# Kernel optimization log

Measured on AMD Instinct MI355X. Metric: run time of the kernel, lower is better.

The kernel has to match this reference:

```python
import jax, jax.numpy as jnp
import numpy as np

N_NODES = 100000
N_EDGES = 3200000
N_GRAPHS = 512
IN_DIM = 128
H1, H2 = 32, 64
OUT_DIM = 1
LN_EPS = 1e-5


def setup_inputs() -> dict:
    key = jax.random.key(0)
    ks = jax.random.split(key, 12)
    x = jax.random.normal(ks[0], (N_NODES, IN_DIM), dtype=jnp.float32)
    edge_index = jax.random.randint(ks[1], (2, N_EDGES), 0, N_NODES, dtype=jnp.int64)
    batch = jnp.sort(jax.random.randint(ks[2], (N_NODES,), 0, N_GRAPHS, dtype=jnp.int64))
    def lin(k, fi, fo):
        s = 1.0 / np.sqrt(fi)
        return jax.random.uniform(k, (fi, fo), minval=-s, maxval=s, dtype=jnp.float32)
    params = {
        'W1': lin(ks[3], IN_DIM, H1), 'b1': jnp.zeros((H1,), jnp.float32),
        'g1': jnp.ones((H1,), jnp.float32), 'be1': jnp.zeros((H1,), jnp.float32),
        'W2': lin(ks[4], H1, H2), 'b2': jnp.zeros((H2,), jnp.float32),
        'g2': jnp.ones((H2,), jnp.float32), 'be2': jnp.zeros((H2,), jnp.float32),
        'Wc1': lin(ks[5], H2, 32), 'bc1': jnp.zeros((32,), jnp.float32),
        'Wc2': lin(ks[6], 32, OUT_DIM), 'bc2': jnp.zeros((OUT_DIM,), jnp.float32),
    }
    return {'x': x, 'edge_index': edge_index, 'batch': batch, **params}


def _gcn_norm(edge_index, n):
    # add self loops (PyG GCNConv default)
    loop = jnp.arange(n, dtype=edge_index.dtype)
    src = jnp.concatenate([edge_index[0], loop])
    dst = jnp.concatenate([edge_index[1], loop])
    deg = jax.ops.segment_sum(jnp.ones_like(dst, dtype=jnp.float32), dst, num_segments=n)
    dinv = jnp.where(deg > 0, 1.0 / jnp.sqrt(deg), 0.0)
    norm = dinv[src] * dinv[dst]  # [E+N]
    return src, dst, norm


def _gcn_conv(x, src, dst, norm, W, b, n):
    h = x @ W                                    # tiny GEMM
    msg = h[src] * norm[:, None]                 # gather + scale (memory-bound)
    agg = jax.ops.segment_sum(msg, dst, num_segments=n)  # scatter-add
    return agg + b


def _layernorm(x, g, b):
    mu = jnp.mean(x, axis=-1, keepdims=True)
    var = jnp.mean(jnp.square(x - mu), axis=-1, keepdims=True)
    return (x - mu) * jax.lax.rsqrt(var + LN_EPS) * g + b


def reference(x, edge_index, batch, W1, b1, g1, be1, W2, b2, g2, be2, Wc1, bc1, Wc2, bc2):
    n = x.shape[0]
    src, dst, norm = _gcn_norm(edge_index, n)
    # layer 1: GCNConv -> LayerNorm -> ReLU (dropout = identity in eval)
    h = jax.nn.relu(_layernorm(_gcn_conv(x, src, dst, norm, W1, b1, n), g1, be1))
    # layer 2
    h = jax.nn.relu(_layernorm(_gcn_conv(h, src, dst, norm, W2, b2, n), g2, be2))
    # global mean pool over graphs
    sums = jax.ops.segment_sum(h, batch, num_segments=N_GRAPHS)
    cnts = jax.ops.segment_sum(jnp.ones((n,), h.dtype), batch, num_segments=N_GRAPHS)
    pooled = sums / jnp.maximum(cnts, 1.0)[:, None]  # [G, H2]
    # classifier MLP
    z = jax.nn.relu(pooled @ Wc1 + bc1)
    return z @ Wc2 + bc2
```

## Files before the change

kernel.cpp:

```cpp
#include <hip/hip_runtime.h>
#include <hip/hip_fp16.h>

#define CAP 10240

__global__ __launch_bounds__(1024) void k_fused1(const int* __restrict__ ei,
                                                 const float* __restrict__ x,
                                                 const float* __restrict__ W1,
                                                 const int* __restrict__ batch,
                                                 int* __restrict__ gcnt,
                                                 int* __restrict__ bucketed,
                                                 __half* __restrict__ hs,
                                                 int* __restrict__ gstart,
                                                 int nA, int nG1, int NB,
                                                 int n, int E, int G) {
    __shared__ __align__(16) char smem[32768];
    int tid = threadIdx.x;
    int bid = blockIdx.x;
    if (bid < nA) {
        int* hist = (int*)smem;
        int* base = (int*)(smem + 2048);
        const int* src = ei;
        const int* dst = ei + E;
        for (int i = tid; i < NB; i += 1024) hist[i] = 0;
        __syncthreads();
        int e0 = bid * 8192;
        int e1 = min(e0 + 8192, E);
        for (int e = e0 + tid; e < e1; e += 1024)
            atomicAdd(&hist[dst[e] >> 8], 1);
        __syncthreads();
        for (int i = tid; i < NB; i += 1024) {
            int h = hist[i];
            base[i] = h ? atomicAdd(&gcnt[i], h) : 0;
            hist[i] = 0;
        }
        __syncthreads();
        for (int e = e0 + tid; e < e1; e += 1024) {
            int d = dst[e], s = src[e];
            int b = d >> 8;
            int p = base[b] + atomicAdd(&hist[b], 1);
            if (p < CAP) bucketed[(size_t)b * CAP + p] = (s << 8) | (d & 255);
        }
    } else if (bid < nA + nG1) {
        float* Ws = (float*)smem;
        float* xs = (float*)(smem + 16384);
        int gb = bid - nA;
        const float4* W4 = (const float4*)W1;
        ((float4*)Ws)[tid] = W4[tid];
        int rbase = gb * 32;
        const float4* x4 = (const float4*)x;
        {
            int r = rbase + (tid >> 5);
            ((float4*)xs)[tid] = (r < n) ? x4[(size_t)r * 32 + (tid & 31)]
                                         : make_float4(0.f, 0.f, 0.f, 0.f);
        }
        __syncthreads();
        int row = tid >> 5, col = tid & 31;
        float acc = 0.0f;
#pragma unroll
        for (int k = 0; k < 128; k++) acc += xs[row * 128 + k] * Ws[k * 32 + col];
        int r = rbase + row;
        if (r < n) hs[(size_t)r * 32 + col] = __float2half(acc);
    } else {
        int i = (bid - nA - nG1) * 1024 + tid;
        if (i > n) return;
        if (i == 0) {
            for (int g = 0; g <= batch[0]; g++) gstart[g] = 0;
        } else if (i == n) {
            for (int g = batch[n - 1] + 1; g <= G; g++) gstart[g] = n;
        } else {
            int b = batch[i], p = batch[i - 1];
            for (int g = p + 1; g <= b; g++) gstart[g] = i;
        }
    }
}

__global__ __launch_bounds__(512) void k_bucketB(const int* __restrict__ bucketed,
                                                 const int* __restrict__ gcnt,
                                                 int* __restrict__ csr,
                                                 int* __restrict__ offs,
                                                 int* __restrict__ deg,
                                                 float* __restrict__ dinv,
                                                 __half* __restrict__ hs, int n) {
    __shared__ int hist[256], scan_a[256], scan_b[256];
    __shared__ float sdinv[256];
    int b = blockIdx.x;
    int tid = threadIdx.x;
    int cnt = min(gcnt[b], CAP);
    int base = b * CAP;
    const int* ent = bucketed + (size_t)b * CAP;
    if (tid < 256) hist[tid] = 0;
    __syncthreads();
    for (int i = tid; i < cnt; i += 512) atomicAdd(&hist[ent[i] & 255], 1);
    __syncthreads();
    int h = (tid < 256) ? hist[tid] : 0;
    if (tid < 256) scan_a[tid] = h;
    __syncthreads();
    int* cur = scan_a;
    int* nxt = scan_b;
    for (int off = 1; off < 256; off <<= 1) {
        if (tid < 256) nxt[tid] = cur[tid] + ((tid >= off) ? cur[tid - off] : 0);
        __syncthreads();
        int* tmp = cur; cur = nxt; nxt = tmp;
    }
    if (tid < 256) {
        int ex = cur[tid] - h;
        float dv = rsqrtf((float)(h + 1));
        sdinv[tid] = dv;
        int node = b * 256 + tid;
        if (node < n) {
            offs[node] = base + ex;
            deg[node] = h;
            dinv[node] = dv;
        }
        hist[tid] = ex;
    }
    __syncthreads();
    for (int i = tid; i < cnt; i += 512) {
        int v = ent[i];
        int p = atomicAdd(&hist[v & 255], 1);
        csr[base + p] = v >> 8;
    }
    float4* hsv = (float4*)hs;
#pragma unroll
    for (int p = 0; p < 2; p++) {
        int idx = p * 512 + tid;
        int nl = idx >> 2, cg = idx & 3;
        int node = b * 256 + nl;
        if (node < n) {
            float dv = sdinv[nl];
            float4 raw = hsv[(size_t)node * 4 + cg];
            __half2* h2 = (__half2*)&raw;
            __half2 o[4];
#pragma unroll
            for (int j = 0; j < 4; j++) {
                float2 f = __half22float2(h2[j]);
                o[j] = __floats2half2_rn(f.x * dv, f.y * dv);
            }
            hsv[(size_t)node * 4 + cg] = *(const float4*)o;
        }
    }
}

template <bool DO_LN>
__global__ __launch_bounds__(256) void k_gather(const __half* __restrict__ hs,
                                                const int* __restrict__ csr,
                                                const int* __restrict__ offs,
                                                const int* __restrict__ deg,
                                                const float* __restrict__ dinv,
                                                const float* __restrict__ b,
                                                const float* __restrict__ g,
                                                const float* __restrict__ be,
                                                __half* __restrict__ out, int n) {
    int wave = threadIdx.x >> 6;
    int lane = threadIdx.x & 63;
    int row = blockIdx.x * 4 + wave;
    if (row >= n) return;
    int nb = lane >> 2;
    int cg = lane & 3;
    int base = offs[row];
    int dg = deg[row];
    const float4* hsv = (const float4*)hs;
    float acc[8];
#pragma unroll
    for (int j = 0; j < 8; j++) acc[j] = 0.f;
    int nfull = dg & ~15;
    for (int it = 0; it < nfull; it += 16) {
        int s = csr[base + it + nb];
        float4 raw = hsv[(size_t)s * 4 + cg];
        const __half2* h2 = (const __half2*)&raw;
#pragma unroll
        for (int j = 0; j < 4; j++) {
            float2 f = __half22float2(h2[j]);
            acc[2 * j]     += f.x;
            acc[2 * j + 1] += f.y;
        }
    }
    if (nfull + nb < dg) {
        int s = csr[base + nfull + nb];
        float4 raw = hsv[(size_t)s * 4 + cg];
        const __half2* h2 = (const __half2*)&raw;
#pragma unroll
        for (int j = 0; j < 4; j++) {
            float2 f = __half22float2(h2[j]);
            acc[2 * j]     += f.x;
            acc[2 * j + 1] += f.y;
        }
    }
#pragma unroll
    for (int m = 4; m <= 32; m <<= 1)
#pragma unroll
        for (int j = 0; j < 8; j++) acc[j] += __shfl_xor(acc[j], m, 64);
    float dv = dinv[row];
    float4 sraw = hsv[(size_t)row * 4 + cg];
    const __half2* sh2 = (const __half2*)&sraw;
    float a[8];
#pragma unroll
    for (int j = 0; j < 4; j++) {
        float2 f = __half22float2(sh2[j]);
        a[2 * j]     = (acc[2 * j]     + f.x) * dv;
        a[2 * j + 1] = (acc[2 * j + 1] + f.y) * dv;
    }
    if (DO_LN) {
        int c0 = cg * 8;
        float s = 0.f;
#pragma unroll
        for (int j = 0; j < 8; j++) { a[j] += b[c0 + j]; s += a[j]; }
#pragma unroll
        for (int m = 1; m <= 2; m <<= 1) s += __shfl_xor(s, m, 64);
        float mu = s * (1.0f / 32.0f);
        float v2 = 0.f;
#pragma unroll
        for (int j = 0; j < 8; j++) { a[j] -= mu; v2 += a[j] * a[j]; }
#pragma unroll
        for (int m = 1; m <= 2; m <<= 1) v2 += __shfl_xor(v2, m, 64);
        float inv = rsqrtf(v2 * (1.0f / 32.0f) + 1e-5f);
#pragma unroll
        for (int j = 0; j < 8; j++)
            a[j] = fmaxf(a[j] * inv * g[c0 + j] + be[c0 + j], 0.f) * dv;
    }
    if (nb == 0) {
        __half2 o[4];
#pragma unroll
        for (int j = 0; j < 4; j++) o[j] = __floats2half2_rn(a[2 * j], a[2 * j + 1]);
        ((float4*)out)[(size_t)row * 4 + cg] = *(const float4*)o;
    }
}

__global__ __launch_bounds__(512) void k_pool_cls(const __half* __restrict__ agg2,
                                                  const float* __restrict__ W2,
                                                  const float* __restrict__ b2,
                                                  const float* __restrict__ g2,
                                                  const float* __restrict__ be2,
                                                  const int* __restrict__ gstart,
                                                  const float* __restrict__ Wc1,
                                                  const float* __restrict__ bc1,
                                                  const float* __restrict__ Wc2,
                                                  const float* __restrict__ bc2,
                                                  float* __restrict__ out) {
    __shared__ float Ws[32 * 64];
    __shared__ float red[8 * 64];
    int tid = threadIdx.x;
    for (int i = tid; i < 32 * 64; i += 512) Ws[i] = W2[i];
    int g = blockIdx.x;
    int r0 = gstart[g], r1 = gstart[g + 1];
    int wave = tid >> 6, lane = tid & 63;
    float pacc = 0.0f;
    __syncthreads();
    for (int row = r0 + wave; row < r1; row += 8) {
        const float4* a4 = (const float4*)(agg2 + (size_t)row * 32);
        float4 r4[4];
#pragma unroll
        for (int q = 0; q < 4; q++) r4[q] = a4[q];
        const __half2* ah = (const __half2*)r4;
        float acc = b2[lane];
#pragma unroll
        for (int k2 = 0; k2 < 16; k2++) {
            float2 f = __half22float2(ah[k2]);
            acc += f.x * Ws[(2 * k2) * 64 + lane] + f.y * Ws[(2 * k2 + 1) * 64 + lane];
        }
        float s = acc;
#pragma unroll
        for (int m = 32; m >= 1; m >>= 1) s += __shfl_xor(s, m, 64);
        float mu = s * (1.0f / 64.0f);
        float d = acc - mu;
        float v = d * d;
#pragma unroll
        for (int m = 32; m >= 1; m >>= 1) v += __shfl_xor(v, m, 64);
        float val = d * rsqrtf(v * (1.0f / 64.0f) + 1e-5f) * g2[lane] + be2[lane];
        pacc += fmaxf(val, 0.0f);
    }
    red[wave * 64 + lane] = pacc;
    __syncthreads();
    if (wave == 0) {
        float p = 0.f;
#pragma unroll
        for (int w = 0; w < 8; w++) p += red[w * 64 + lane];
        p *= 1.0f / fmaxf((float)(r1 - r0), 1.0f);
        red[lane] = p;
    }
    __syncthreads();
    if (wave == 0 && lane < 32) {
        float zs = bc1[lane];
#pragma unroll
        for (int k = 0; k < 64; k++) zs += red[k] * Wc1[k * 32 + lane];
        float o = fmaxf(zs, 0.0f) * Wc2[lane];
#pragma unroll
        for (int m = 16; m >= 1; m >>= 1) o += __shfl_xor(o, m, 64);
        if (lane == 0) out[g] = o + bc2[0];
    }
}


extern "C" void kernel_launch(void* const* d_in, const int* in_sizes, int n_in,
                              void* d_out, int out_size, void* d_ws, size_t ws_size,
                              hipStream_t stream) {
    const float* x     = (const float*)d_in[0];
    const int*   ei    = (const int*)d_in[1];
    const int*   batch = (const int*)d_in[2];
    const float* W1  = (const float*)d_in[3];
    const float* b1  = (const float*)d_in[4];
    const float* g1  = (const float*)d_in[5];
    const float* be1 = (const float*)d_in[6];
    const float* W2  = (const float*)d_in[7];
    const float* b2  = (const float*)d_in[8];
    const float* g2  = (const float*)d_in[9];
    const float* be2 = (const float*)d_in[10];
    const float* Wc1 = (const float*)d_in[11];
    const float* bc1 = (const float*)d_in[12];
    const float* Wc2 = (const float*)d_in[13];
    const float* bc2 = (const float*)d_in[14];

    int n = in_sizes[0] / 128;
    int E = in_sizes[1] / 2;
    int G = out_size;
    int NB = (n + 255) >> 8;

    float* ws     = (float*)d_ws;
    float* dinv   = ws;
    int*   deg    = (int*)(dinv + n);
    int*   offs   = deg + n;
    int*   gcnt   = offs + n;
    int*   gstart = gcnt + 512;
    int*   csr    = gstart + 516;
    __half* hsA   = (__half*)(csr + (size_t)NB * CAP);
    int*   bucketed = (int*)(hsA + (size_t)n * 32);
    __half* hsB   = (__half*)bucketed;

    int nA  = (E + 8191) / 8192;
    int nG1 = (n + 31) / 32;
    int nGs = (n + 1024) / 1024;

    hipMemsetAsync(gcnt, 0, NB * sizeof(int), stream);

    k_fused1<<<nA + nG1 + nGs, 1024, 0, stream>>>(ei, x, W1, batch, gcnt, bucketed,
                                                  hsA, gstart, nA, nG1, NB, n, E, G);
    k_bucketB<<<NB, 512, 0, stream>>>(bucketed, gcnt, csr, offs, deg, dinv, hsA, n);

    k_gather<true><<<(n + 3) / 4, 256, 0, stream>>>(hsA, csr, offs, deg, dinv,
                                                    b1, g1, be1, hsB, n);
    k_gather<false><<<(n + 3) / 4, 256, 0, stream>>>(hsB, csr, offs, deg, dinv,
                                                     nullptr, nullptr, nullptr, hsA, n);
    k_pool_cls<<<G, 512, 0, stream>>>(hsA, W2, b2, g2, be2, gstart,
                                      Wc1, bc1, Wc2, bc2, (float*)d_out);
}
```

Before: 234.7 us.

## Split CSR by source half to improve gather cache locality; restructure X@W1

Each destination's neighbor list is now split into two segments, by whether the source index falls in the lower or upper half of the nodes. Each GCN layer's gather then runs as two passes, each touching only half of the fp16 feature table, so that working set has a better chance of staying in L2. The first pass writes a partial sum, and the second pass adds it back before normalization and LayerNorm. The first-layer GEMM is rewritten so each thread computes four outputs of a row, streaming x from global memory instead of staging it in shared memory. CAP and the shared-memory size are also reduced. The cost is two extra kernel launches, an extra partial-sum write and read per layer, and more warp divergence from the masked gather loop.

```diff
diff --git a/kernel.cpp b/kernel.cpp
--- a/kernel.cpp
+++ b/kernel.cpp
@@ -1,7 +1,7 @@
 #include <hip/hip_runtime.h>
 #include <hip/hip_fp16.h>
 
-#define CAP 10240
+#define CAP 9216
 
 __global__ __launch_bounds__(1024) void k_fused1(const int* __restrict__ ei,
                                                  const float* __restrict__ x,
@@ -13,7 +13,7 @@
                                                  int* __restrict__ gstart,
                                                  int nA, int nG1, int NB,
                                                  int n, int E, int G) {
-    __shared__ __align__(16) char smem[32768];
+    __shared__ __align__(16) char smem[16384];
     int tid = threadIdx.x;
     int bid = blockIdx.x;
     if (bid < nA) {
@@ -42,24 +42,28 @@
         }
     } else if (bid < nA + nG1) {
         float* Ws = (float*)smem;
-        float* xs = (float*)(smem + 16384);
-        int gb = bid - nA;
         const float4* W4 = (const float4*)W1;
         ((float4*)Ws)[tid] = W4[tid];
-        int rbase = gb * 32;
+        __syncthreads();
+        int gb = bid - nA;
+        int row = gb * 128 + (tid >> 3);
+        int g8 = tid & 7;
+        if (row >= n) return;
         const float4* x4 = (const float4*)x;
-        {
-            int r = rbase + (tid >> 5);
-            ((float4*)xs)[tid] = (r < n) ? x4[(size_t)r * 32 + (tid & 31)]
-                                         : make_float4(0.f, 0.f, 0.f, 0.f);
-        }
-        __syncthreads();
-        int row = tid >> 5, col = tid & 31;
-        float acc = 0.0f;
-#pragma unroll
-        for (int k = 0; k < 128; k++) acc += xs[row * 128 + k] * Ws[k * 32 + col];
-        int r = rbase + row;
-        if (r < n) hs[(size_t)r * 32 + col] = __float2half(acc);
+        const float4* Ws4 = (const float4*)Ws;
+        float a0 = 0.f, a1 = 0.f, a2 = 0.f, a3 = 0.f;
+#pragma unroll 4
+        for (int j = 0; j < 32; j++) {
+            float4 xq = x4[(size_t)row * 32 + j];
+#pragma unroll
+            for (int t = 0; t < 4; t++) {
+                float xv = (t == 0) ? xq.x : (t == 1) ? xq.y : (t == 2) ? xq.z : xq.w;
+                float4 wv = Ws4[(4 * j + t) * 8 + g8];
+                a0 += xv * wv.x; a1 += xv * wv.y; a2 += xv * wv.z; a3 += xv * wv.w;
+            }
+        }
+        __half2 o[2] = { __floats2half2_rn(a0, a1), __floats2half2_rn(a2, a3) };
+        *(float2*)(hs + (size_t)row * 32 + g8 * 4) = *(const float2*)o;
     } else {
         int i = (bid - nA - nG1) * 1024 + tid;
         if (i > n) return;
@@ -78,46 +82,56 @@
                                                  const int* __restrict__ gcnt,
                                                  int* __restrict__ csr,
                                                  int* __restrict__ offs,
+                                                 int* __restrict__ offsh,
                                                  int* __restrict__ deg,
                                                  float* __restrict__ dinv,
-                                                 __half* __restrict__ hs, int n) {
-    __shared__ int hist[256], scan_a[256], scan_b[256];
+                                                 __half* __restrict__ hs,
+                                                 int n, int nh) {
+    __shared__ int hist[512], hcnt[512], scan_a[512], scan_b[512];
     __shared__ float sdinv[256];
     int b = blockIdx.x;
     int tid = threadIdx.x;
     int cnt = min(gcnt[b], CAP);
     int base = b * CAP;
     const int* ent = bucketed + (size_t)b * CAP;
-    if (tid < 256) hist[tid] = 0;
-    __syncthreads();
-    for (int i = tid; i < cnt; i += 512) atomicAdd(&hist[ent[i] & 255], 1);
-    __syncthreads();
-    int h = (tid < 256) ? hist[tid] : 0;
-    if (tid < 256) scan_a[tid] = h;
+    hist[tid] = 0;
+    __syncthreads();
+    for (int i = tid; i < cnt; i += 512) {
+        int v = ent[i];
+        int key = (v & 255) | (((v >> 8) >= nh) ? 256 : 0);
+        atomicAdd(&hist[key], 1);
+    }
+    __syncthreads();
+    int h = hist[tid];
+    hcnt[tid] = h;
+    scan_a[tid] = h;
     __syncthreads();
     int* cur = scan_a;
     int* nxt = scan_b;
-    for (int off = 1; off < 256; off <<= 1) {
-        if (tid < 256) nxt[tid] = cur[tid] + ((tid >= off) ? cur[tid - off] : 0);
+    for (int off = 1; off < 512; off <<= 1) {
+        nxt[tid] = cur[tid] + ((tid >= off) ? cur[tid - off] : 0);
         __syncthreads();
         int* tmp = cur; cur = nxt; nxt = tmp;
     }
+    hist[tid] = cur[tid] - hcnt[tid];
     if (tid < 256) {
-        int ex = cur[tid] - h;
-        float dv = rsqrtf((float)(h + 1));
+        int dlo = hcnt[tid];
+        int dhi = hcnt[256 + tid];
+        float dv = rsqrtf((float)(dlo + dhi + 1));
         sdinv[tid] = dv;
         int node = b * 256 + tid;
         if (node < n) {
-            offs[node] = base + ex;
-            deg[node] = h;
-            dinv[node] = dv;
-        }
-        hist[tid] = ex;
+            offs[node]  = base + cur[tid] - dlo;
+            offsh[node] = base + cur[256 + tid] - dhi;
+            deg[node]   = dlo | (dhi << 16);
+            dinv[node]  = dv;
+        }
     }
     __syncthreads();
     for (int i = tid; i < cnt; i += 512) {
         int v = ent[i];
-        int p = atomicAdd(&hist[v & 255], 1);
+        int key = (v & 255) | (((v >> 8) >= nh) ? 256 : 0);
+        int p = atomicAdd(&hist[key], 1);
         csr[base + p] = v >> 8;
     }
     float4* hsv = (float4*)hs;
@@ -141,16 +155,11 @@
     }
 }
 
-template <bool DO_LN>
-__global__ __launch_bounds__(256) void k_gather(const __half* __restrict__ hs,
-                                                const int* __restrict__ csr,
-                                                const int* __restrict__ offs,
-                                                const int* __restrict__ deg,
-                                                const float* __restrict__ dinv,
-                                                const float* __restrict__ b,
-                                                const float* __restrict__ g,
-                                                const float* __restrict__ be,
-                                                __half* __restrict__ out, int n) {
+__global__ __launch_bounds__(256) void k_gatherA(const __half* __restrict__ hs,
+                                                 const int* __restrict__ csr,
+                                                 const int* __restrict__ offs,
+                                                 const int* __restrict__ deg,
+                                                 __half* __restrict__ out, int n) {
     int wave = threadIdx.x >> 6;
     int lane = threadIdx.x & 63;
     int row = blockIdx.x * 4 + wave;
@@ -158,32 +167,71 @@
     int nb = lane >> 2;
     int cg = lane & 3;
     int base = offs[row];
-    int dg = deg[row];
+    int dg = deg[row] & 0xffff;
     const float4* hsv = (const float4*)hs;
     float acc[8];
 #pragma unroll
     for (int j = 0; j < 8; j++) acc[j] = 0.f;
-    int nfull = dg & ~15;
-    for (int it = 0; it < nfull; it += 16) {
-        int s = csr[base + it + nb];
-        float4 raw = hsv[(size_t)s * 4 + cg];
-        const __half2* h2 = (const __half2*)&raw;
-#pragma unroll
-        for (int j = 0; j < 4; j++) {
-            float2 f = __half22float2(h2[j]);
-            acc[2 * j]     += f.x;
-            acc[2 * j + 1] += f.y;
-        }
-    }
-    if (nfull + nb < dg) {
-        int s = csr[base + nfull + nb];
-        float4 raw = hsv[(size_t)s * 4 + cg];
-        const __half2* h2 = (const __half2*)&raw;
-#pragma unroll
-        for (int j = 0; j < 4; j++) {
-            float2 f = __half22float2(h2[j]);
-            acc[2 * j]     += f.x;
-            acc[2 * j + 1] += f.y;
+    for (int it = 0; it < dg; it += 16) {
+        int e = it + nb;
+        if (e < dg) {
+            int s = csr[base + e];
+            float4 raw = hsv[(size_t)s * 4 + cg];
+            const __half2* h2 = (const __half2*)&raw;
+#pragma unroll
+            for (int j = 0; j < 4; j++) {
+                float2 f = __half22float2(h2[j]);
+                acc[2 * j]     += f.x;
+                acc[2 * j + 1] += f.y;
+            }
+        }
+    }
+#pragma unroll
+    for (int m = 4; m <= 32; m <<= 1)
+#pragma unroll
+        for (int j = 0; j < 8; j++) acc[j] += __shfl_xor(acc[j], m, 64);
+    if (nb == 0) {
+        __half2 o[4];
+#pragma unroll
+        for (int j = 0; j < 4; j++) o[j] = __floats2half2_rn(acc[2 * j], acc[2 * j + 1]);
+        ((float4*)out)[(size_t)row * 4 + cg] = *(const float4*)o;
+    }
+}
+
+template <bool DO_LN>
+__global__ __launch_bounds__(256) void k_gatherB(const __half* __restrict__ hs,
+                                                 const int* __restrict__ csr,
+                                                 const int* __restrict__ offsh,
+                                                 const int* __restrict__ deg,
+                                                 const float* __restrict__ dinv,
+                                                 const float* __restrict__ b,
+                                                 const float* __restrict__ g,
+                                                 const float* __restrict__ be,
+                                                 __half* __restrict__ out, int n) {
+    int wave = threadIdx.x >> 6;
+    int lane = threadIdx.x & 63;
+    int row = blockIdx.x * 4 + wave;
+    if (row >= n) return;
+    int nb = lane >> 2;
+    int cg = lane & 3;
+    int base = offsh[row];
+    int dg = deg[row] >> 16;
+    const float4* hsv = (const float4*)hs;
+    float acc[8];
+#pragma unroll
+    for (int j = 0; j < 8; j++) acc[j] = 0.f;
+    for (int it = 0; it < dg; it += 16) {
+        int e = it + nb;
+        if (e < dg) {
+            int s = csr[base + e];
+            float4 raw = hsv[(size_t)s * 4 + cg];
+            const __half2* h2 = (const __half2*)&raw;
+#pragma unroll
+            for (int j = 0; j < 4; j++) {
+                float2 f = __half22float2(h2[j]);
+                acc[2 * j]     += f.x;
+                acc[2 * j + 1] += f.y;
+            }
         }
     }
 #pragma unroll
@@ -192,13 +240,16 @@
         for (int j = 0; j < 8; j++) acc[j] += __shfl_xor(acc[j], m, 64);
     float dv = dinv[row];
     float4 sraw = hsv[(size_t)row * 4 + cg];
+    float4 praw = ((const float4*)out)[(size_t)row * 4 + cg];
     const __half2* sh2 = (const __half2*)&sraw;
+    const __half2* ph2 = (const __half2*)&praw;
     float a[8];
 #pragma unroll
     for (int j = 0; j < 4; j++) {
-        float2 f = __half22float2(sh2[j]);
-        a[2 * j]     = (acc[2 * j]     + f.x) * dv;
-        a[2 * j + 1] = (acc[2 * j + 1] + f.y) * dv;
+        float2 fs = __half22float2(sh2[j]);
+        float2 fp = __half22float2(ph2[j]);
+        a[2 * j]     = (acc[2 * j]     + fs.x + fp.x) * dv;
+        a[2 * j + 1] = (acc[2 * j + 1] + fs.y + fp.y) * dv;
     }
     if (DO_LN) {
         int c0 = cg * 8;
@@ -314,12 +365,14 @@
     int E = in_sizes[1] / 2;
     int G = out_size;
     int NB = (n + 255) >> 8;
+    int nh = n >> 1;
 
     float* ws     = (float*)d_ws;
     float* dinv   = ws;
     int*   deg    = (int*)(dinv + n);
     int*   offs   = deg + n;
-    int*   gcnt   = offs + n;
+    int*   offsh  = offs + n;
+    int*   gcnt   = offsh + n;
     int*   gstart = gcnt + 512;
     int*   csr    = gstart + 516;
     __half* hsA   = (__half*)(csr + (size_t)NB * CAP);
@@ -327,19 +380,22 @@
     __half* hsB   = (__half*)bucketed;
 
     int nA  = (E + 8191) / 8192;
-    int nG1 = (n + 31) / 32;
+    int nG1 = (n + 127) / 128;
     int nGs = (n + 1024) / 1024;
 
     hipMemsetAsync(gcnt, 0, NB * sizeof(int), stream);
 
     k_fused1<<<nA + nG1 + nGs, 1024, 0, stream>>>(ei, x, W1, batch, gcnt, bucketed,
                                                   hsA, gstart, nA, nG1, NB, n, E, G);
-    k_bucketB<<<NB, 512, 0, stream>>>(bucketed, gcnt, csr, offs, deg, dinv, hsA, n);
-
-    k_gather<true><<<(n + 3) / 4, 256, 0, stream>>>(hsA, csr, offs, deg, dinv,
-                                                    b1, g1, be1, hsB, n);
-    k_gather<false><<<(n + 3) / 4, 256, 0, stream>>>(hsB, csr, offs, deg, dinv,
-                                                     nullptr, nullptr, nullptr, hsA, n);
+    k_bucketB<<<NB, 512, 0, stream>>>(bucketed, gcnt, csr, offs, offsh, deg,
+                                      dinv, hsA, n, nh);
+
+    k_gatherA<<<(n + 3) / 4, 256, 0, stream>>>(hsA, csr, offs, deg, hsB, n);
+    k_gatherB<true><<<(n + 3) / 4, 256, 0, stream>>>(hsA, csr, offsh, deg, dinv,
+                                                     b1, g1, be1, hsB, n);
+    k_gatherA<<<(n + 3) / 4, 256, 0, stream>>>(hsB, csr, offs, deg, hsA, n);
+    k_gatherB<false><<<(n + 3) / 4, 256, 0, stream>>>(hsB, csr, offsh, deg, dinv,
+                                                      nullptr, nullptr, nullptr, hsA, n);
     k_pool_cls<<<G, 512, 0, stream>>>(hsA, W2, b2, g2, be2, gstart,
                                       Wc1, bc1, Wc2, bc2, (float*)d_out);
 }
```

New measurement: 275.4 us. 17.3% more time.

## Stage bucketed edges in LDS before global write and restructure X@W1 GEMM

Applied to the files above, without the earlier changes.

The edge-bucketing blocks now keep each edge's dst and src in registers, prefix-sum the per-bucket histogram, and sort edges into an LDS buffer by bucket. They then write each bucket's run to global memory as a contiguous stretch, which replaces scattered per-edge global writes and the second global read of the edge arrays. The first-layer GEMM blocks now process 128 rows each. Every thread computes 4 output columns straight from global x using float4 weights in LDS and stores packed halves. The bucket count is hardcoded to 512, and the copy-out has one thread per bucket walking its run serially, which may leave write coalescing poor.

```diff
diff --git a/kernel.cpp b/kernel.cpp
--- a/kernel.cpp
+++ b/kernel.cpp
@@ -13,53 +13,89 @@
                                                  int* __restrict__ gstart,
                                                  int nA, int nG1, int NB,
                                                  int n, int E, int G) {
-    __shared__ __align__(16) char smem[32768];
+    __shared__ __align__(16) char smem[40960];
     int tid = threadIdx.x;
     int bid = blockIdx.x;
     if (bid < nA) {
         int* hist = (int*)smem;
-        int* base = (int*)(smem + 2048);
+        int* excl = hist + 512;
+        int* gb   = excl + 512;
+        int* ebuf = gb + 512;
         const int* src = ei;
         const int* dst = ei + E;
-        for (int i = tid; i < NB; i += 1024) hist[i] = 0;
+        for (int i = tid; i < 512; i += 1024) hist[i] = 0;
         __syncthreads();
         int e0 = bid * 8192;
-        int e1 = min(e0 + 8192, E);
-        for (int e = e0 + tid; e < e1; e += 1024)
-            atomicAdd(&hist[dst[e] >> 8], 1);
-        __syncthreads();
-        for (int i = tid; i < NB; i += 1024) {
-            int h = hist[i];
-            base[i] = h ? atomicAdd(&gcnt[i], h) : 0;
-            hist[i] = 0;
-        }
-        __syncthreads();
-        for (int e = e0 + tid; e < e1; e += 1024) {
-            int d = dst[e], s = src[e];
-            int b = d >> 8;
-            int p = base[b] + atomicAdd(&hist[b], 1);
-            if (p < CAP) bucketed[(size_t)b * CAP + p] = (s << 8) | (d & 255);
+        int d[8], sR[8];
+#pragma unroll
+        for (int k = 0; k < 8; k++) {
+            int e = e0 + k * 1024 + tid;
+            bool v = e < E;
+            d[k]  = v ? dst[e] : -1;
+            sR[k] = v ? src[e] : 0;
+            if (v) atomicAdd(&hist[d[k] >> 8], 1);
+        }
+        __syncthreads();
+        if (tid < 512) excl[tid] = hist[tid];
+        __syncthreads();
+        for (int off = 1; off < 512; off <<= 1) {
+            int v2 = 0;
+            if (tid < 512) v2 = excl[tid] + ((tid >= off) ? excl[tid - off] : 0);
+            __syncthreads();
+            if (tid < 512) excl[tid] = v2;
+            __syncthreads();
+        }
+        if (tid < 512) {
+            int c = hist[tid];
+            int ex = excl[tid] - c;
+            excl[tid] = ex;
+            gb[tid] = c ? atomicAdd(&gcnt[tid], c) : 0;
+            hist[tid] = ex;
+        }
+        __syncthreads();
+#pragma unroll
+        for (int k = 0; k < 8; k++) {
+            if (d[k] >= 0) {
+                int b = d[k] >> 8;
+                int p = atomicAdd(&hist[b], 1);
+                ebuf[p] = (sR[k] << 8) | (d[k] & 255);
+            }
+        }
+        __syncthreads();
+        if (tid < 512) {
+            int lds0 = excl[tid];
+            int cnt  = hist[tid] - lds0;
+            int gb0  = gb[tid];
+            int* dstp = bucketed + (size_t)tid * CAP;
+            for (int k = 0; k < cnt; k++) {
+                int gp = gb0 + k;
+                if (gp < CAP) dstp[gp] = ebuf[lds0 + k];
+            }
         }
     } else if (bid < nA + nG1) {
         float* Ws = (float*)smem;
-        float* xs = (float*)(smem + 16384);
-        int gb = bid - nA;
         const float4* W4 = (const float4*)W1;
         ((float4*)Ws)[tid] = W4[tid];
-        int rbase = gb * 32;
+        __syncthreads();
+        int gb2 = bid - nA;
+        int row = gb2 * 128 + (tid >> 3);
+        int g8 = tid & 7;
+        if (row >= n) return;
         const float4* x4 = (const float4*)x;
-        {
-            int r = rbase + (tid >> 5);
-            ((float4*)xs)[tid] = (r < n) ? x4[(size_t)r * 32 + (tid & 31)]
-                                         : make_float4(0.f, 0.f, 0.f, 0.f);
-        }
-        __syncthreads();
-        int row = tid >> 5, col = tid & 31;
-        float acc = 0.0f;
-#pragma unroll
-        for (int k = 0; k < 128; k++) acc += xs[row * 128 + k] * Ws[k * 32 + col];
-        int r = rbase + row;
-        if (r < n) hs[(size_t)r * 32 + col] = __float2half(acc);
+        const float4* Ws4 = (const float4*)Ws;
+        float a0 = 0.f, a1 = 0.f, a2 = 0.f, a3 = 0.f;
+#pragma unroll 4
+        for (int j = 0; j < 32; j++) {
+            float4 xq = x4[(size_t)row * 32 + j];
+#pragma unroll
+            for (int t = 0; t < 4; t++) {
+                float xv = (t == 0) ? xq.x : (t == 1) ? xq.y : (t == 2) ? xq.z : xq.w;
+                float4 wv = Ws4[(4 * j + t) * 8 + g8];
+                a0 += xv * wv.x; a1 += xv * wv.y; a2 += xv * wv.z; a3 += xv * wv.w;
+            }
+        }
+        __half2 o[2] = { __floats2half2_rn(a0, a1), __floats2half2_rn(a2, a3) };
+        *(float2*)(hs + (size_t)row * 32 + g8 * 4) = *(const float2*)o;
     } else {
         int i = (bid - nA - nG1) * 1024 + tid;
         if (i > n) return;
@@ -327,10 +363,10 @@
     __half* hsB   = (__half*)bucketed;
 
     int nA  = (E + 8191) / 8192;
-    int nG1 = (n + 31) / 32;
+    int nG1 = (n + 127) / 128;
     int nGs = (n + 1024) / 1024;
 
-    hipMemsetAsync(gcnt, 0, NB * sizeof(int), stream);
+    hipMemsetAsync(gcnt, 0, 512 * sizeof(int), stream);
 
     k_fused1<<<nA + nG1 + nGs, 1024, 0, stream>>>(ei, x, W1, batch, gcnt, bucketed,
                                                   hsA, gstart, nA, nG1, NB, n, E, G);
```

Measured after the change: 217.4 us. 7.4% less time.
